# Kernel optimization log

Measured on AMD Instinct MI355X. Metric: run time of the kernel, lower is better.

The kernel has to match this reference:

```python
import jax, jax.numpy as jnp
import numpy as np

D_MODEL = 1024
N_HEADS = 16
D_HEAD = 64
NEG = -1000000000.0


def setup_inputs() -> dict:
    key = jax.random.key(0)
    k1, k2, k3 = jax.random.split(key, 3)
    B, T = 2, 2048
    x = jax.random.normal(k1, (B, T, D_MODEL), dtype=jnp.float32)
    # qkv_proj: Linear(d_model, 3*H*D, bias=False) -> weight (3*H*D, d_model)
    w_qkv = jax.random.normal(k2, (3 * N_HEADS * D_HEAD, D_MODEL), dtype=jnp.float32) * (D_MODEL ** -0.5)
    # o_proj: Linear(H*D, d_model, bias=False) -> weight (d_model, H*D)
    w_o = jax.random.normal(k3, (D_MODEL, N_HEADS * D_HEAD), dtype=jnp.float32) * ((N_HEADS * D_HEAD) ** -0.5)
    return {"x": x, "w_qkv": w_qkv, "w_o": w_o}


def reference(x, w_qkv, w_o):
    B, T, _ = x.shape
    H, D = N_HEADS, D_HEAD
    scale = D ** -0.5
    qkv = jnp.einsum('btm,nm->btn', x, w_qkv).reshape(B, T, 3, H, D)
    q, k, v = qkv[:, :, 0], qkv[:, :, 1], qkv[:, :, 2]  # (B,T,H,D)
    # scores: (B,H,T,T)
    attn = jnp.einsum('bqhd,bkhd->bhqk', q, k) * scale
    causal = jnp.tril(jnp.ones((T, T), dtype=x.dtype))
    attn = attn + (1.0 - causal) * NEG
    attn = jax.nn.softmax(attn, axis=-1)
    out = jnp.einsum('bhqk,bkhd->bqhd', attn, v).reshape(B, T, H * D)
    out = jnp.einsum('btn,mn->btm', out, w_o)
    return (out, k, v)
```

## Files before the change

kernel.cpp:

```cpp
#include <hip/hip_runtime.h>
#include <cstdint>

typedef unsigned short u16;
typedef __bf16 bf16x8 __attribute__((ext_vector_type(8)));
typedef float f32x4 __attribute__((ext_vector_type(4)));
typedef short s4 __attribute__((ext_vector_type(4)));

#define T_SEQ 2048
#define NH 16

__device__ __forceinline__ u16 f2bf(float f) {
  union { float f; uint32_t u; } x; x.f = f;
  uint32_t r = (x.u + 0x7fffu + ((x.u >> 16) & 1u)) >> 16;
  return (u16)r;
}

__device__ __forceinline__ uint32_t pk2bf(float a, float b) {
  union { float f; uint32_t u; } x, y; x.f = a; y.f = b;
  uint32_t lo = (x.u + 0x7fffu + ((x.u >> 16) & 1u)) >> 16;
  uint32_t hi = (y.u + 0x7fffu + ((y.u >> 16) & 1u)) >> 16;
  return lo | (hi << 16);
}

__device__ __forceinline__ void cvt8(u16* dst, const float* src) {
  float4 a = *(const float4*)src;
  float4 b = *(const float4*)(src + 4);
  uint4 o;
  o.x = pk2bf(a.x, a.y); o.y = pk2bf(a.z, a.w);
  o.z = pk2bf(b.x, b.y); o.w = pk2bf(b.z, b.w);
  *(uint4*)dst = o;
}

__global__ __launch_bounds__(256) void cvt_all(const float* __restrict__ x,
                                               const float* __restrict__ wq,
                                               const float* __restrict__ wo,
                                               u16* __restrict__ dst) {
  int i = blockIdx.x * 256 + threadIdx.x;
  const float* src; int off;
  if (i < 524288)      { src = x;  off = 0; }
  else if (i < 917504) { src = wq; off = 524288; }
  else                 { src = wo; off = 917504; }
  cvt8(&dst[(size_t)i * 8], &src[(size_t)(i - off) * 8]);
}

__device__ __forceinline__ s4 cvt4(f32x4 v) {
  union { __bf16 b[4]; s4 s; } u;
  u.b[0] = (__bf16)v[0]; u.b[1] = (__bf16)v[1];
  u.b[2] = (__bf16)v[2]; u.b[3] = (__bf16)v[3];
  return u.s;
}

__device__ __forceinline__ f32x4 mfma16(s4 a, s4 b, f32x4 c) {
#if __has_builtin(__builtin_amdgcn_mfma_f32_16x16x16bf16_1k)
  return __builtin_amdgcn_mfma_f32_16x16x16bf16_1k(a, b, c, 0, 0, 0);
#else
  asm("v_mfma_f32_16x16x16_bf16 %0, %1, %2, %0" : "+v"(c) : "v"(a), "v"(b));
  return c;
#endif
}

__device__ __forceinline__ float exp2fast(float x) {
#if __has_builtin(__builtin_amdgcn_exp2f)
  return __builtin_amdgcn_exp2f(x);
#else
  float r; asm("v_exp_f32 %0, %1" : "=v"(r) : "v"(x)); return r;
#endif
}

__device__ __forceinline__ void gl_lds(const u16* g, u16* ldsbase) {
  __builtin_amdgcn_global_load_lds(
      (const __attribute__((address_space(1))) void*)g,
      (__attribute__((address_space(3))) void*)ldsbase, 16, 0, 0);
}

template <bool CF32, bool KV, int WAVES>
__global__ __launch_bounds__(WAVES * 64) void gemm_bt(
    const u16* __restrict__ A, const u16* __restrict__ W,
    void* __restrict__ Cp, float* __restrict__ outk, float* __restrict__ outv,
    int M, int N, int K) {
  constexpr int NJ = (WAVES == 4) ? 4 : 2;
  constexpr int SI = 16 / WAVES;
  __shared__ __align__(16) u16 As[128 * 64];
  __shared__ __align__(16) u16 Bs[128 * 64];
  const int tid  = threadIdx.x;
  const int bid  = blockIdx.y * gridDim.x + blockIdx.x;
  const int per  = (gridDim.x * gridDim.y) >> 3;
  const int swz  = (bid & 7) * per + (bid >> 3);
  const int n0   = (swz % gridDim.x) * 128;
  const int m0   = (swz / gridDim.x) * 128;
  const int lane = tid & 63;
  const int wave = tid >> 6;
  const int wm   = (WAVES == 4 ? (wave >> 1) : (wave >> 2)) * 64;
  const int wn   = (WAVES == 4 ? (wave & 1) * 64 : (wave & 3) * 32);
  const int l15  = lane & 15;
  const int quad = lane >> 4;
  const int srow = lane >> 3;
  const int sc   = lane & 7;

  f32x4 acc[4][NJ];
#pragma unroll
  for (int i = 0; i < 4; i++)
#pragma unroll
    for (int j = 0; j < NJ; j++) acc[i][j] = (f32x4){0.f, 0.f, 0.f, 0.f};

  for (int k0 = 0; k0 < K; k0 += 64) {
    __syncthreads();
#pragma unroll
    for (int i = 0; i < SI; i++) {
      int r0  = (i * WAVES + wave) * 8;
      int row = r0 + srow;
      int gc  = (sc ^ (row & 7)) << 3;
      gl_lds(&A[(size_t)(m0 + row) * K + k0 + gc], &As[r0 * 64]);
      gl_lds(&W[(size_t)(n0 + row) * K + k0 + gc], &Bs[r0 * 64]);
    }
    __syncthreads();
#pragma unroll
    for (int kk = 0; kk < 64; kk += 32) {
      bf16x8 af[4], bfr[NJ];
#pragma unroll
      for (int i = 0; i < 4; i++) {
        int arow = wm + i * 16 + l15;
        af[i] = *(const bf16x8*)((const char*)As + arow * 128 +
                                 ((((kk >> 3) + quad) ^ (arow & 7)) << 4));
      }
#pragma unroll
      for (int j = 0; j < NJ; j++) {
        int brow = wn + j * 16 + l15;
        bfr[j] = *(const bf16x8*)((const char*)Bs + brow * 128 +
                                  ((((kk >> 3) + quad) ^ (brow & 7)) << 4));
      }
#pragma unroll
      for (int i = 0; i < 4; i++)
#pragma unroll
        for (int j = 0; j < NJ; j++)
          acc[i][j] = __builtin_amdgcn_mfma_f32_16x16x32_bf16(af[i], bfr[j], acc[i][j], 0, 0, 0);
    }
  }
#pragma unroll
  for (int i = 0; i < 4; i++)
#pragma unroll
    for (int j = 0; j < NJ; j++)
#pragma unroll
      for (int r = 0; r < 4; r++) {
        int row = m0 + wm + i * 16 + quad * 4 + r;
        int col = n0 + wn + j * 16 + l15;
        float v = acc[i][j][r];
        if constexpr (CF32) {
          ((float*)Cp)[(size_t)row * N + col] = v;
        } else {
          ((u16*)Cp)[(size_t)row * N + col] = f2bf(v);
          if constexpr (KV) {
            if (col >= 2048)      outv[(size_t)row * 1024 + (col - 2048)] = v;
            else if (col >= 1024) outk[(size_t)row * 1024 + (col - 1024)] = v;
          }
        }
      }
}

__global__ __launch_bounds__(256) void transpose_v(const u16* __restrict__ qkv,
                                                   u16* __restrict__ vt) {
  __shared__ __align__(16) u16 tile[64 * 72];
  int t0 = blockIdx.x * 64;
  int bh = blockIdx.y;
  int b = bh >> 4, h = bh & 15;
  int tid = threadIdx.x;
  int t8 = tid & 7, rowb = tid >> 3;
#pragma unroll
  for (int r = 0; r < 2; r++) {
    int row = rowb + r * 32;
    *(uint4*)&tile[row * 72 + t8 * 8] =
        *(const uint4*)&qkv[((size_t)b * T_SEQ + t0 + row) * 3072 + 2048 + h * 64 + t8 * 8];
  }
  __syncthreads();
#pragma unroll
  for (int r = 0; r < 2; r++) {
    int d = rowb + r * 32;
    union { u16 s[8]; uint4 u; } tmp;
#pragma unroll
    for (int e = 0; e < 8; e++) tmp.s[e] = tile[(t8 * 8 + e) * 72 + d];
    *(uint4*)&vt[((size_t)(b * NH + h) * 64 + d) * 2048 + t0 + t8 * 8] = tmp.u;
  }
}

__global__ __launch_bounds__(256) void attn(const u16* __restrict__ qkv,
                                            const u16* __restrict__ vt,
                                            u16* __restrict__ o) {
  __shared__ __align__(16) u16 Ks[3][64 * 64];
  __shared__ __align__(16) u16 Vts[3][64 * 64];

  const int tid  = threadIdx.x;
  const int pair = blockIdx.x;
  const int bh   = blockIdx.y;
  const int b    = bh >> 4, h = bh & 15;
  const int lane = tid & 63, wave = tid >> 6;
  const int l15  = lane & 15, quad = lane >> 4;
  const int srow = lane >> 3, sc = lane & 7;
  const size_t qbase = (size_t)b * T_SEQ * 3072;
  const size_t vbase = (size_t)(b * NH + h) * 64 * 2048;
  const float C = 0.1803368801f;

  const int qtA = pair, qtB = 31 - pair;
  const int wq0A = qtA * 64 + wave * 16;
  const int wq0B = qtB * 64 + wave * 16;
  const u16* qpA = &qkv[qbase + (size_t)(wq0A + l15) * 3072 + h * 64];
  const u16* qpB = &qkv[qbase + (size_t)(wq0B + l15) * 3072 + h * 64];
  bf16x8 qf0 = *(const bf16x8*)&qpA[quad * 8];
  bf16x8 qf1 = *(const bf16x8*)&qpA[32 + quad * 8];
  const bf16x8 qB0 = *(const bf16x8*)&qpB[quad * 8];
  const bf16x8 qB1 = *(const bf16x8*)&qpB[32 + quad * 8];

  int qt = qtA, wq0 = wq0A, qrow = wq0A + l15;

  f32x4 acc_o[4];
#pragma unroll
  for (int n = 0; n < 4; n++) acc_o[n] = (f32x4){0.f, 0.f, 0.f, 0.f};
  float m2run = -1e30f, lrun = 0.f;

  auto ktof = [&](int s) { return (s > pair) ? (s - pair - 1) : s; };

  auto stage = [&](int buf, int s) {
    const int k0 = ktof(s) * 64;
#pragma unroll
    for (int i = 0; i < 2; i++) {
      int r0  = (wave * 2 + i) * 8;
      int row = r0 + srow;
      int gc  = (sc ^ (row & 7)) << 3;
      gl_lds(&qkv[qbase + (size_t)(k0 + row) * 3072 + 1024 + h * 64 + gc], &Ks[buf][r0 * 64]);
      gl_lds(&vt[vbase + (size_t)row * 2048 + k0 + gc], &Vts[buf][r0 * 64]);
    }
  };

  auto writeout = [&]() {
    float linv = 1.0f / lrun;
#pragma unroll
    for (int r = 0; r < 4; r++) {
      float lr = __shfl(linv, quad * 4 + r);
      int row = wq0 + quad * 4 + r;
#pragma unroll
      for (int n = 0; n < 4; n++)
        o[(size_t)(b * T_SEQ + row) * 1024 + h * 64 + n * 16 + l15] =
            f2bf(acc_o[n][r] * lr);
    }
  };

  stage(0, 0);
  stage(1, 1);

  const int steps = 33;
  for (int s = 0; s < steps; s++) {
    if (s < steps - 1) asm volatile("s_waitcnt vmcnt(4)" ::: "memory");
    else               asm volatile("s_waitcnt vmcnt(0)" ::: "memory");
    __builtin_amdgcn_s_barrier();
    __builtin_amdgcn_sched_barrier(0);

    if (s + 2 < steps) stage((s + 2) % 3, s + 2);

    if (s == pair + 1) {
      writeout();
#pragma unroll
      for (int n = 0; n < 4; n++) acc_o[n] = (f32x4){0.f, 0.f, 0.f, 0.f};
      m2run = -1e30f; lrun = 0.f;
      qt = qtB; wq0 = wq0B; qrow = wq0B + l15;
      qf0 = qB0; qf1 = qB1;
    }

    const int cur = s % 3;
    const int kt  = ktof(s);
    const int k0  = kt * 64;

    f32x4 sacc[4];
#pragma unroll
    for (int j = 0; j < 4; j++) sacc[j] = (f32x4){0.f, 0.f, 0.f, 0.f};
#pragma unroll
    for (int j = 0; j < 4; j++) {
      int krow = j * 16 + l15;
      const char* kb = (const char*)&Ks[cur][0] + krow * 128;
      bf16x8 kfa = *(const bf16x8*)(kb + ((quad ^ (krow & 7)) << 4));
      bf16x8 kfb = *(const bf16x8*)(kb + (((4 + quad) ^ (krow & 7)) << 4));
      sacc[j] = __builtin_amdgcn_mfma_f32_16x16x32_bf16(kfa, qf0, sacc[j], 0, 0, 0);
      sacc[j] = __builtin_amdgcn_mfma_f32_16x16x32_bf16(kfb, qf1, sacc[j], 0, 0, 0);
    }

    if (kt == qt) {
#pragma unroll
      for (int j = 0; j < 4; j++)
#pragma unroll
        for (int r = 0; r < 4; r++) {
          int k = k0 + j * 16 + quad * 4 + r;
          if (k > qrow) sacc[j][r] = -1e30f;
        }
    }

    float mj[4];
#pragma unroll
    for (int j = 0; j < 4; j++)
      mj[j] = fmaxf(fmaxf(sacc[j][0], sacc[j][1]), fmaxf(sacc[j][2], sacc[j][3]));
    float mx = fmaxf(fmaxf(mj[0], mj[1]), fmaxf(mj[2], mj[3]));
    mx = fmaxf(mx, __shfl_xor(mx, 16));
    mx = fmaxf(mx, __shfl_xor(mx, 32));
    const float m2x = mx * C;

    if (!__all(m2x <= m2run + 8.0f)) {
      const float m2new = fmaxf(m2run, m2x);
      const float alpha = exp2fast(m2run - m2new);
      lrun *= alpha;
      m2run = m2new;
#pragma unroll
      for (int r = 0; r < 4; r++) {
        float ar = __shfl(alpha, quad * 4 + r);
#pragma unroll
        for (int n = 0; n < 4; n++) acc_o[n][r] *= ar;
      }
    }

    const float nm = m2run;
    float ts[4];
#pragma unroll
    for (int j = 0; j < 4; j++) {
#pragma unroll
      for (int r = 0; r < 4; r++) sacc[j][r] = exp2fast(fmaf(sacc[j][r], C, -nm));
      ts[j] = (sacc[j][0] + sacc[j][1]) + (sacc[j][2] + sacc[j][3]);
    }
    float sum = (ts[0] + ts[1]) + (ts[2] + ts[3]);
    sum += __shfl_xor(sum, 16);
    sum += __shfl_xor(sum, 32);
    lrun += sum;

    s4 pa[4];
#pragma unroll
    for (int j = 0; j < 4; j++) pa[j] = cvt4(sacc[j]);

#pragma unroll
    for (int j = 0; j < 4; j++)
#pragma unroll
      for (int n = 0; n < 4; n++) {
        int vrow = n * 16 + l15;
        int ch = (j * 2 + (quad >> 1)) ^ (vrow & 7);
        const s4 vf = *(const s4*)((const char*)&Vts[cur][0] + vrow * 128 +
                                   (ch << 4) + ((quad & 1) << 3));
        acc_o[n] = mfma16(pa[j], vf, acc_o[n]);
      }
  }

  writeout();
}

extern "C" void kernel_launch(void* const* d_in, const int* in_sizes, int n_in,
                              void* d_out, int out_size, void* d_ws, size_t ws_size,
                              hipStream_t stream) {
  const float* x     = (const float*)d_in[0];
  const float* w_qkv = (const float*)d_in[1];
  const float* w_o   = (const float*)d_in[2];
  float* out  = (float*)d_out;
  float* outk = out + (size_t)4194304;
  float* outv = out + (size_t)8388608;

  u16* qkv = (u16*)d_ws;
  u16* vt  = qkv + (size_t)4096 * 3072;
  u16* ao  = vt  + (size_t)4194304;
  u16* xb  = ao  + (size_t)4194304;
  u16* wqb = xb  + (size_t)4194304;
  u16* wob = wqb + (size_t)3145728;

  cvt_all<<<4096, 256, 0, stream>>>(x, w_qkv, w_o, xb);

  gemm_bt<false, true, 4><<<dim3(24, 32), 256, 0, stream>>>(
      xb, wqb, qkv, outk, outv, 4096, 3072, 1024);
  transpose_v<<<dim3(32, 32), 256, 0, stream>>>(qkv, vt);
  attn<<<dim3(16, 32), 256, 0, stream>>>(qkv, vt, ao);
  gemm_bt<true, false, 8><<<dim3(8, 32), 512, 0, stream>>>(
      ao, wob, out, nullptr, nullptr, 4096, 1024, 1024);
}
```

Baseline: 211.0 us.

## Fuse V transpose into QKV GEMM epilogue and load V fragments directly to registers

The QKV projection GEMM epilogue now writes the V columns straight into the transposed bf16 layout, so the separate transpose_v kernel and its launch go away. Inside attention, V tiles are no longer staged through LDS. Each wave loads its V fragments from global memory into registers at the top of every step. The vmcnt waits are moved to just before the PV MFMAs, and s_setprio is raised around the MFMA blocks. This removes a kernel, some LDS traffic and LDS footprint, at the cost of uncoalesced 8-byte V loads and more register pressure in attention.

```diff
diff --git a/kernel.cpp b/kernel.cpp
--- a/kernel.cpp
+++ b/kernel.cpp
@@ -77,7 +77,7 @@
 __global__ __launch_bounds__(WAVES * 64) void gemm_bt(
     const u16* __restrict__ A, const u16* __restrict__ W,
     void* __restrict__ Cp, float* __restrict__ outk, float* __restrict__ outv,
-    int M, int N, int K) {
+    u16* __restrict__ vtp, int M, int N, int K) {
   constexpr int NJ = (WAVES == 4) ? 4 : 2;
   constexpr int SI = 16 / WAVES;
   __shared__ __align__(16) u16 As[128 * 64];
@@ -139,54 +139,40 @@
 #pragma unroll
   for (int i = 0; i < 4; i++)
 #pragma unroll
-    for (int j = 0; j < NJ; j++)
-#pragma unroll
-      for (int r = 0; r < 4; r++) {
-        int row = m0 + wm + i * 16 + quad * 4 + r;
-        int col = n0 + wn + j * 16 + l15;
-        float v = acc[i][j][r];
-        if constexpr (CF32) {
-          ((float*)Cp)[(size_t)row * N + col] = v;
-        } else {
-          ((u16*)Cp)[(size_t)row * N + col] = f2bf(v);
+    for (int j = 0; j < NJ; j++) {
+      const int row0 = m0 + wm + i * 16 + quad * 4;
+      const int col  = n0 + wn + j * 16 + l15;
+      if constexpr (CF32) {
+#pragma unroll
+        for (int r = 0; r < 4; r++)
+          ((float*)Cp)[(size_t)(row0 + r) * N + col] = acc[i][j][r];
+      } else if (KV && col >= 2048) {
+        const int hd = col - 2048;
+        const int b_ = row0 >> 11, t_ = row0 & 2047;
+        uint2 pk;
+        pk.x = pk2bf(acc[i][j][0], acc[i][j][1]);
+        pk.y = pk2bf(acc[i][j][2], acc[i][j][3]);
+        *(uint2*)&vtp[((size_t)(b_ * NH + (hd >> 6)) * 64 + (hd & 63)) * 2048 + t_] = pk;
+#pragma unroll
+        for (int r = 0; r < 4; r++)
+          outv[(size_t)(row0 + r) * 1024 + hd] = acc[i][j][r];
+      } else {
+#pragma unroll
+        for (int r = 0; r < 4; r++) {
+          float v = acc[i][j][r];
+          ((u16*)Cp)[(size_t)(row0 + r) * N + col] = f2bf(v);
           if constexpr (KV) {
-            if (col >= 2048)      outv[(size_t)row * 1024 + (col - 2048)] = v;
-            else if (col >= 1024) outk[(size_t)row * 1024 + (col - 1024)] = v;
+            if (col >= 1024) outk[(size_t)(row0 + r) * 1024 + (col - 1024)] = v;
           }
         }
       }
-}
-
-__global__ __launch_bounds__(256) void transpose_v(const u16* __restrict__ qkv,
-                                                   u16* __restrict__ vt) {
-  __shared__ __align__(16) u16 tile[64 * 72];
-  int t0 = blockIdx.x * 64;
-  int bh = blockIdx.y;
-  int b = bh >> 4, h = bh & 15;
-  int tid = threadIdx.x;
-  int t8 = tid & 7, rowb = tid >> 3;
-#pragma unroll
-  for (int r = 0; r < 2; r++) {
-    int row = rowb + r * 32;
-    *(uint4*)&tile[row * 72 + t8 * 8] =
-        *(const uint4*)&qkv[((size_t)b * T_SEQ + t0 + row) * 3072 + 2048 + h * 64 + t8 * 8];
-  }
-  __syncthreads();
-#pragma unroll
-  for (int r = 0; r < 2; r++) {
-    int d = rowb + r * 32;
-    union { u16 s[8]; uint4 u; } tmp;
-#pragma unroll
-    for (int e = 0; e < 8; e++) tmp.s[e] = tile[(t8 * 8 + e) * 72 + d];
-    *(uint4*)&vt[((size_t)(b * NH + h) * 64 + d) * 2048 + t0 + t8 * 8] = tmp.u;
-  }
+    }
 }
 
 __global__ __launch_bounds__(256) void attn(const u16* __restrict__ qkv,
                                             const u16* __restrict__ vt,
                                             u16* __restrict__ o) {
   __shared__ __align__(16) u16 Ks[3][64 * 64];
-  __shared__ __align__(16) u16 Vts[3][64 * 64];
 
   const int tid  = threadIdx.x;
   const int pair = blockIdx.x;
@@ -209,6 +195,11 @@
   const bf16x8 qB0 = *(const bf16x8*)&qpB[quad * 8];
   const bf16x8 qB1 = *(const bf16x8*)&qpB[32 + quad * 8];
 
+  const u16* vp[4];
+#pragma unroll
+  for (int n = 0; n < 4; n++)
+    vp[n] = &vt[vbase + (size_t)(n * 16 + l15) * 2048 + quad * 4];
+
   int qt = qtA, wq0 = wq0A, qrow = wq0A + l15;
 
   f32x4 acc_o[4];
@@ -226,7 +217,6 @@
       int row = r0 + srow;
       int gc  = (sc ^ (row & 7)) << 3;
       gl_lds(&qkv[qbase + (size_t)(k0 + row) * 3072 + 1024 + h * 64 + gc], &Ks[buf][r0 * 64]);
-      gl_lds(&vt[vbase + (size_t)row * 2048 + k0 + gc], &Vts[buf][r0 * 64]);
     }
   };
 
@@ -245,13 +235,22 @@
 
   stage(0, 0);
   stage(1, 1);
+  asm volatile("s_waitcnt vmcnt(2)" ::: "memory");
 
   const int steps = 33;
   for (int s = 0; s < steps; s++) {
-    if (s < steps - 1) asm volatile("s_waitcnt vmcnt(4)" ::: "memory");
-    else               asm volatile("s_waitcnt vmcnt(0)" ::: "memory");
     __builtin_amdgcn_s_barrier();
     __builtin_amdgcn_sched_barrier(0);
+
+    const int kt = ktof(s);
+    const int k0 = kt * 64;
+
+    s4 vreg[4][4];
+#pragma unroll
+    for (int j = 0; j < 4; j++)
+#pragma unroll
+      for (int n = 0; n < 4; n++)
+        vreg[j][n] = *(const s4*)(vp[n] + k0 + j * 16);
 
     if (s + 2 < steps) stage((s + 2) % 3, s + 2);
 
@@ -265,12 +264,11 @@
     }
 
     const int cur = s % 3;
-    const int kt  = ktof(s);
-    const int k0  = kt * 64;
 
     f32x4 sacc[4];
 #pragma unroll
     for (int j = 0; j < 4; j++) sacc[j] = (f32x4){0.f, 0.f, 0.f, 0.f};
+    __builtin_amdgcn_s_setprio(1);
 #pragma unroll
     for (int j = 0; j < 4; j++) {
       int krow = j * 16 + l15;
@@ -280,6 +278,7 @@
       sacc[j] = __builtin_amdgcn_mfma_f32_16x16x32_bf16(kfa, qf0, sacc[j], 0, 0, 0);
       sacc[j] = __builtin_amdgcn_mfma_f32_16x16x32_bf16(kfb, qf1, sacc[j], 0, 0, 0);
     }
+    __builtin_amdgcn_s_setprio(0);
 
     if (kt == qt) {
 #pragma unroll
@@ -330,16 +329,17 @@
 #pragma unroll
     for (int j = 0; j < 4; j++) pa[j] = cvt4(sacc[j]);
 
+    if (s + 2 < steps) asm volatile("s_waitcnt vmcnt(2)" ::: "memory");
+    else               asm volatile("s_waitcnt vmcnt(0)" ::: "memory");
+    __builtin_amdgcn_sched_barrier(0);
+
+    __builtin_amdgcn_s_setprio(1);
 #pragma unroll
     for (int j = 0; j < 4; j++)
 #pragma unroll
-      for (int n = 0; n < 4; n++) {
-        int vrow = n * 16 + l15;
-        int ch = (j * 2 + (quad >> 1)) ^ (vrow & 7);
-        const s4 vf = *(const s4*)((const char*)&Vts[cur][0] + vrow * 128 +
-                                   (ch << 4) + ((quad & 1) << 3));
-        acc_o[n] = mfma16(pa[j], vf, acc_o[n]);
-      }
+      for (int n = 0; n < 4; n++)
+        acc_o[n] = mfma16(pa[j], vreg[j][n], acc_o[n]);
+    __builtin_amdgcn_s_setprio(0);
   }
 
   writeout();
@@ -365,9 +365,8 @@
   cvt_all<<<4096, 256, 0, stream>>>(x, w_qkv, w_o, xb);
 
   gemm_bt<false, true, 4><<<dim3(24, 32), 256, 0, stream>>>(
-      xb, wqb, qkv, outk, outv, 4096, 3072, 1024);
-  transpose_v<<<dim3(32, 32), 256, 0, stream>>>(qkv, vt);
+      xb, wqb, qkv, outk, outv, vt, 4096, 3072, 1024);
   attn<<<dim3(16, 32), 256, 0, stream>>>(qkv, vt, ao);
   gemm_bt<true, false, 8><<<dim3(8, 32), 512, 0, stream>>>(
-      ao, wob, out, nullptr, nullptr, 4096, 1024, 1024);
-}
+      ao, wob, out, nullptr, nullptr, nullptr, 4096, 1024, 1024);
+}
```

New measurement: 279.7 us. +32.6%, slower.
